# Optimization experiments

Hardware: AMD Instinct MI355X
Metric: run time of the kernel (lower is better)

The kernel has to match this reference:

```python
import jax, jax.numpy as jnp
import numpy as np

HID = 1152      # vision_hidden_size
HEADS = 16      # vision_num_heads
HD = HID // HEADS  # 72
INTER = 4304    # vision_intermediate_size
SEQ = 16384     # total vision tokens
WIN = 64        # tokens per attention window
EPS = 1e-6


def setup_inputs() -> dict:
    key = jax.random.key(0)
    ks = jax.random.split(key, 14)
    f32 = jnp.float32
    x = jax.random.normal(ks[0], (SEQ, HID), f32)
    # RoPE tables: standard rotary angles, full head_dim via concat(ang, ang)
    inv_freq = 1.0 / (10000.0 ** (jnp.arange(0, HD // 2, dtype=f32) / (HD // 2)))
    ang = jnp.arange(SEQ, dtype=f32)[:, None] * inv_freq[None, :]
    emb = jnp.concatenate([ang, ang], axis=-1)          # [SEQ, HD]
    cos, sin = jnp.cos(emb), jnp.sin(emb)
    cu_seqlens = jnp.arange(SEQ // WIN + 1, dtype=jnp.int32) * WIN  # uniform windows
    sc = 0.02
    return {
        "x": x, "cos": cos, "sin": sin, "cu_seqlens": cu_seqlens,
        "qkv_w": jax.random.normal(ks[1], (HID, 3 * HID), f32) * sc,
        "qkv_b": jnp.zeros((3 * HID,), f32),
        "proj_w": jax.random.normal(ks[2], (HID, HID), f32) * sc,
        "proj_b": jnp.zeros((HID,), f32),
        "ln1_w": jnp.ones((HID,), f32), "ln1_b": jnp.zeros((HID,), f32),
        "ln2_w": jnp.ones((HID,), f32), "ln2_b": jnp.zeros((HID,), f32),
        "fc1_w": jax.random.normal(ks[3], (HID, INTER), f32) * sc,
        "fc1_b": jnp.zeros((INTER,), f32),
        "fc2_w": jax.random.normal(ks[4], (INTER, HID), f32) * sc,
        "fc2_b": jnp.zeros((HID,), f32),
    }


def _layer_norm(h, w, b):
    hf = h.astype(jnp.float32)
    mean = jnp.mean(hf, axis=-1, keepdims=True)
    var = jnp.mean((hf - mean) ** 2, axis=-1, keepdims=True)
    return ((hf - mean) * jax.lax.rsqrt(var + EPS)) * w + b


def _rotate_half(t):
    t1, t2 = jnp.split(t, 2, axis=-1)
    return jnp.concatenate((-t2, t1), axis=-1)


def reference(x, cos, sin, cu_seqlens,
              qkv_w, qkv_b, proj_w, proj_b,
              ln1_w, ln1_b, ln2_w, ln2_b,
              fc1_w, fc1_b, fc2_w, fc2_b):
    S = x.shape[0]
    n_win = cu_seqlens.shape[0] - 1
    W = S // n_win  # uniform windows (block-diagonal attention)

    # --- attention branch ---
    h = _layer_norm(x, ln1_w, ln1_b)
    qkv = h @ qkv_w + qkv_b
    q, k, v = jnp.split(qkv, 3, axis=-1)
    q = q.reshape(S, HEADS, HD)
    k = k.reshape(S, HEADS, HD)
    v = v.reshape(S, HEADS, HD)
    c = cos[:, None, :HD]
    s = sin[:, None, :HD]
    q = q * c + _rotate_half(q) * s
    k = k * c + _rotate_half(k) * s
    # block-diagonal windowed attention: [n_win, W, HEADS, HD]
    qw = q.reshape(n_win, W, HEADS, HD).astype(jnp.float32)
    kw = k.reshape(n_win, W, HEADS, HD).astype(jnp.float32)
    vw = v.reshape(n_win, W, HEADS, HD).astype(jnp.float32)
    scores = jnp.einsum('wqhd,wkhd->whqk', qw, kw) * (HD ** -0.5)
    probs = jax.nn.softmax(scores, axis=-1)
    out = jnp.einsum('whqk,wkhd->wqhd', probs, vw).reshape(S, HID)
    x = x + (out @ proj_w + proj_b)

    # --- MLP branch ---
    h2 = _layer_norm(x, ln2_w, ln2_b)
    m = jax.nn.gelu(h2 @ fc1_w + fc1_b, approximate=True)
    return x + (m @ fc2_w + fc2_b)
```

## Files before the change

### kernel.cpp

```cpp
#include <hip/hip_runtime.h>
#include <stdint.h>


#define SEQ   16384
#define HID   1152
#define NH    16
#define HDIM  72
#define INTER 4304
#define INTERP 4352
#define QKVN  3456

using bf16x8 = __attribute__((ext_vector_type(8))) __bf16;
using f32x4  = __attribute__((ext_vector_type(4))) float;

__device__ __forceinline__ float bf2f(uint16_t u){ return __uint_as_float(((uint32_t)u)<<16); }
__device__ __forceinline__ uint16_t f2bf(float f){
  uint32_t u = __float_as_uint(f);
  u += 0x7fffu + ((u>>16)&1u);
  return (uint16_t)(u>>16);
}
__device__ __forceinline__ float gelu_tanh(float x){
  float t = tanhf(0.7978845608028654f*(x + 0.044715f*x*x*x));
  return 0.5f*x*(1.0f + t);
}
__device__ __forceinline__ void async_load16(const void* g, void* l){
  __builtin_amdgcn_global_load_lds((__attribute__((address_space(1))) void*)(void*)g,
                                   (__attribute__((address_space(3))) void*)l, 16, 0, 0);
}

__global__ void transpose_cast(const float* __restrict__ src, uint16_t* __restrict__ dst,
                               int R, int C, int Rp)
{
  __shared__ float tile[32][33];
  const int tx = threadIdx.x & 31, ty = threadIdx.x >> 5;
  const int c = blockIdx.x*32 + tx;
  #pragma unroll
  for (int s = 0; s < 4; ++s){
    const int r = blockIdx.y*32 + ty + s*8;
    tile[ty + s*8][tx] = (r < R && c < C) ? src[(size_t)r*C + c] : 0.0f;
  }
  __syncthreads();
  #pragma unroll
  for (int s = 0; s < 4; ++s){
    const int oc = blockIdx.x*32 + ty + s*8;
    const int orr = blockIdx.y*32 + tx;
    dst[(size_t)oc*Rp + orr] = f2bf(tile[tx][ty + s*8]);
  }
}

__global__ void ln_kernel(const float* __restrict__ x, const float* __restrict__ w,
                          const float* __restrict__ b, uint16_t* __restrict__ out)
{
  const int wid = threadIdx.x >> 6, lane = threadIdx.x & 63;
  const int row = blockIdx.x*4 + wid;
  const float* xr = x + (size_t)row*HID;
  float v[18];
  float s = 0.f;
  #pragma unroll
  for (int t = 0; t < 18; ++t){ v[t] = xr[lane + t*64]; s += v[t]; }
  #pragma unroll
  for (int m = 32; m; m >>= 1) s += __shfl_xor(s, m, 64);
  const float mean = s * (1.0f/HID);
  float q = 0.f;
  #pragma unroll
  for (int t = 0; t < 18; ++t){ float d = v[t]-mean; q += d*d; }
  #pragma unroll
  for (int m = 32; m; m >>= 1) q += __shfl_xor(q, m, 64);
  const float rstd = rsqrtf(q*(1.0f/HID) + 1e-6f);
  uint16_t* orow = out + (size_t)row*HID;
  #pragma unroll
  for (int t = 0; t < 18; ++t){
    const int j = lane + t*64;
    orow[j] = f2bf((v[t]-mean)*rstd*w[j] + b[j]);
  }
}

__global__ void rope_kernel(uint16_t* __restrict__ qkv, const float* __restrict__ cosb,
                            const float* __restrict__ sinb)
{
  const int idx = blockIdx.x*256 + threadIdx.x;
  const int s  = idx / (NH*36);
  const int r1 = idx - s*(NH*36);
  const int h  = r1 / 36;
  const int d  = r1 - h*36;
  const float c  = cosb[s*HDIM + d];
  const float sn = sinb[s*HDIM + d];
  const size_t b = (size_t)s*QKVN + h*HDIM + d;
  float q1 = bf2f(qkv[b]), q2 = bf2f(qkv[b+36]);
  qkv[b]    = f2bf(q1*c - q2*sn);
  qkv[b+36] = f2bf(q2*c + q1*sn);
  float k1 = bf2f(qkv[b+HID]), k2 = bf2f(qkv[b+HID+36]);
  qkv[b+HID]    = f2bf(k1*c - k2*sn);
  qkv[b+HID+36] = f2bf(k2*c + k1*sn);
}

__global__ __launch_bounds__(256,2) void attn_kernel(const uint16_t* __restrict__ qkv,
                                                     uint16_t* __restrict__ outb)
{
  __shared__ float Q[64*76];
  __shared__ float K[64*76];
  __shared__ float V[64*76];
  __shared__ float P[64*68];
  const int tid = threadIdx.x;
  const int win = blockIdx.x >> 4, h = blockIdx.x & 15;
  const size_t base = (size_t)win*64*QKVN + h*HDIM;
  {
    const int r = tid >> 2, q4 = tid & 3;
    const size_t rb = base + (size_t)r*QKVN;
    #pragma unroll
    for (int p0 = 0; p0 < 9; ++p0){
      const int p = q4*9 + p0;
      const uint32_t uq = *(const uint32_t*)(qkv + rb + 2*p);
      const uint32_t uk = *(const uint32_t*)(qkv + rb + HID + 2*p);
      const uint32_t uv = *(const uint32_t*)(qkv + rb + 2*HID + 2*p);
      Q[r*76+2*p] = bf2f((uint16_t)uq); Q[r*76+2*p+1] = bf2f((uint16_t)(uq>>16));
      K[r*76+2*p] = bf2f((uint16_t)uk); K[r*76+2*p+1] = bf2f((uint16_t)(uk>>16));
      V[r*76+2*p] = bf2f((uint16_t)uv); V[r*76+2*p+1] = bf2f((uint16_t)(uv>>16));
    }
  }
  __syncthreads();
  const int rg = tid >> 4, cg = tid & 15;
  const int r0 = rg*4, c0 = cg*4;
  float sc[4][4] = {};
  #pragma unroll 3
  for (int kk = 0; kk < 18; ++kk){
    float4 qv[4], kv[4];
    #pragma unroll
    for (int i = 0; i < 4; ++i) qv[i] = *(const float4*)&Q[(r0+i)*76 + kk*4];
    #pragma unroll
    for (int j = 0; j < 4; ++j) kv[j] = *(const float4*)&K[(c0+j)*76 + kk*4];
    #pragma unroll
    for (int i = 0; i < 4; ++i)
      #pragma unroll
      for (int j = 0; j < 4; ++j)
        sc[i][j] += qv[i].x*kv[j].x + qv[i].y*kv[j].y + qv[i].z*kv[j].z + qv[i].w*kv[j].w;
  }
  const float scale = 0.11785113019775793f;
  #pragma unroll
  for (int i = 0; i < 4; ++i){
    float a0 = sc[i][0]*scale, a1 = sc[i][1]*scale, a2 = sc[i][2]*scale, a3 = sc[i][3]*scale;
    float m = fmaxf(fmaxf(a0,a1), fmaxf(a2,a3));
    m = fmaxf(m, __shfl_xor(m, 1, 16));
    m = fmaxf(m, __shfl_xor(m, 2, 16));
    m = fmaxf(m, __shfl_xor(m, 4, 16));
    m = fmaxf(m, __shfl_xor(m, 8, 16));
    float e0 = __expf(a0-m), e1 = __expf(a1-m), e2 = __expf(a2-m), e3 = __expf(a3-m);
    float sm = e0+e1+e2+e3;
    sm += __shfl_xor(sm, 1, 16);
    sm += __shfl_xor(sm, 2, 16);
    sm += __shfl_xor(sm, 4, 16);
    sm += __shfl_xor(sm, 8, 16);
    const float inv = 1.0f/sm;
    *(float4*)&P[(r0+i)*68 + c0] = make_float4(e0*inv, e1*inv, e2*inv, e3*inv);
  }
  __syncthreads();
  for (int d4 = cg; d4 < 18; d4 += 16){
    float4 o[4] = {};
    #pragma unroll 4
    for (int k4 = 0; k4 < 16; ++k4){
      float4 pr[4];
      #pragma unroll
      for (int i = 0; i < 4; ++i) pr[i] = *(const float4*)&P[(r0+i)*68 + k4*4];
      const float4 v0 = *(const float4*)&V[(k4*4+0)*76 + d4*4];
      const float4 v1 = *(const float4*)&V[(k4*4+1)*76 + d4*4];
      const float4 v2 = *(const float4*)&V[(k4*4+2)*76 + d4*4];
      const float4 v3 = *(const float4*)&V[(k4*4+3)*76 + d4*4];
      #pragma unroll
      for (int i = 0; i < 4; ++i){
        o[i].x += pr[i].x*v0.x + pr[i].y*v1.x + pr[i].z*v2.x + pr[i].w*v3.x;
        o[i].y += pr[i].x*v0.y + pr[i].y*v1.y + pr[i].z*v2.y + pr[i].w*v3.y;
        o[i].z += pr[i].x*v0.z + pr[i].y*v1.z + pr[i].z*v2.z + pr[i].w*v3.z;
        o[i].w += pr[i].x*v0.w + pr[i].y*v1.w + pr[i].z*v2.w + pr[i].w*v3.w;
      }
    }
    #pragma unroll
    for (int i = 0; i < 4; ++i){
      const int token = win*64 + r0 + i;
      const size_t ob = (size_t)token*HID + h*HDIM + d4*4;
      outb[ob+0] = f2bf(o[i].x); outb[ob+1] = f2bf(o[i].y);
      outb[ob+2] = f2bf(o[i].z); outb[ob+3] = f2bf(o[i].w);
    }
  }
}

template<int EPI>
__global__ __launch_bounds__(256,3) void gemm_bt(
    const uint16_t* __restrict__ A, const uint16_t* __restrict__ Bt,
    const float* __restrict__ bias, int Nb,
    const float* res, void* outp, int N, int K, int NB)
{
  __shared__ uint16_t sA[128*64];
  __shared__ uint16_t sB[128*64];
  const int tid = threadIdx.x, wid = tid >> 6, lane = tid & 63;
  const int per  = gridDim.x >> 3;
  const int tile = (blockIdx.x & 7)*per + (blockIdx.x >> 3);
  const int mb   = tile / NB;
  const int mBase = mb*128, nBase = (tile - mb*NB)*128;
  const int wm = wid >> 1, wn = wid & 1;
  const int sr = lane >> 2;
  const int sk = lane & 3;
  const int gk = sk ^ ((sr >> 1) & 3);
  const int rr = lane & 15;
  const int rq = lane >> 4;
  const int rp = rq ^ ((rr >> 1) & 3);
  f32x4 acc[4][4] = {};

  for (int k0 = 0; k0 < K; k0 += 64){
    __syncthreads();
    #pragma unroll
    for (int j = 0; j < 4; ++j){
      const int c  = wid*4 + j;
      const int rc = c >> 1, h = c & 1;
      const size_t gcol = (size_t)(k0 + h*32 + gk*8);
      async_load16(A  + (size_t)(mBase + rc*16 + sr)*K + gcol, &sA[c*512]);
      async_load16(Bt + (size_t)(nBase + rc*16 + sr)*K + gcol, &sB[c*512]);
    }
    __syncthreads();
    #pragma unroll
    for (int h = 0; h < 2; ++h){
      bf16x8 af[4], bfr[4];
      #pragma unroll
      for (int i = 0; i < 4; ++i)
        af[i] = *(const bf16x8*)&sA[((wm*4 + i)*2 + h)*512 + rr*32 + rp*8];
      #pragma unroll
      for (int j = 0; j < 4; ++j)
        bfr[j] = *(const bf16x8*)&sB[((wn*4 + j)*2 + h)*512 + rr*32 + rp*8];
      #pragma unroll
      for (int i = 0; i < 4; ++i)
        #pragma unroll
        for (int j = 0; j < 4; ++j)
          acc[i][j] = __builtin_amdgcn_mfma_f32_16x16x32_bf16(af[i], bfr[j], acc[i][j], 0, 0, 0);
    }
  }

  const int rqd = (lane>>4)*4, cl = lane & 15;
  #pragma unroll
  for (int i = 0; i < 4; ++i){
    #pragma unroll
    for (int j = 0; j < 4; ++j){
      const int col = nBase + wn*64 + j*16 + cl;
      const float bv = (col < Nb) ? bias[col] : 0.0f;
      #pragma unroll
      for (int r = 0; r < 4; ++r){
        const int row = mBase + wm*64 + i*16 + rqd + r;
        const float v = acc[i][j][r] + bv;
        const size_t o = (size_t)row*N + col;
        if (EPI == 0)      ((uint16_t*)outp)[o] = f2bf(v);
        else if (EPI == 1) ((uint16_t*)outp)[o] = f2bf(gelu_tanh(v));
        else               ((float*)outp)[o] = v + res[o];
      }
    }
  }
}

extern "C" void kernel_launch(void* const* d_in, const int* in_sizes, int n_in,
                              void* d_out, int out_size, void* d_ws, size_t ws_size,
                              hipStream_t stream)
{
  const float* x      = (const float*)d_in[0];
  const float* cosb   = (const float*)d_in[1];
  const float* sinb   = (const float*)d_in[2];
  const float* qkv_w  = (const float*)d_in[4];
  const float* qkv_b  = (const float*)d_in[5];
  const float* proj_w = (const float*)d_in[6];
  const float* proj_b = (const float*)d_in[7];
  const float* ln1_w  = (const float*)d_in[8];
  const float* ln1_b  = (const float*)d_in[9];
  const float* ln2_w  = (const float*)d_in[10];
  const float* ln2_b  = (const float*)d_in[11];
  const float* fc1_w  = (const float*)d_in[12];
  const float* fc1_b  = (const float*)d_in[13];
  const float* fc2_w  = (const float*)d_in[14];
  const float* fc2_b  = (const float*)d_in[15];

  char* ws = (char*)d_ws;
  uint16_t* Wqkv  = (uint16_t*)(ws + 0);
  uint16_t* Wproj = (uint16_t*)(ws + 7962624);
  uint16_t* Wfc1  = (uint16_t*)(ws + 10616832);
  uint16_t* Wfc2  = (uint16_t*)(ws + 20643840);
  uint16_t* Hbuf  = (uint16_t*)(ws + 30670848);
  uint16_t* QKV   = (uint16_t*)(ws + 68419584);
  uint16_t* MB    = QKV;
  float* X1 = (float*)d_out;

  transpose_cast<<<dim3(108,36), 256, 0, stream>>>(qkv_w, Wqkv, 1152, 3456, 1152);
  transpose_cast<<<dim3(36,36),  256, 0, stream>>>(proj_w, Wproj, 1152, 1152, 1152);
  transpose_cast<<<dim3(136,36), 256, 0, stream>>>(fc1_w, Wfc1, 1152, 4304, 1152);
  transpose_cast<<<dim3(36,136), 256, 0, stream>>>(fc2_w, Wfc2, 4304, 1152, 4352);

  ln_kernel<<<4096, 256, 0, stream>>>(x, ln1_w, ln1_b, Hbuf);
  gemm_bt<0><<<27*128, 256, 0, stream>>>(Hbuf, Wqkv, qkv_b, QKVN, nullptr, QKV, QKVN, HID, 27);
  rope_kernel<<<36864, 256, 0, stream>>>(QKV, cosb, sinb);
  attn_kernel<<<4096, 256, 0, stream>>>(QKV, Hbuf);
  gemm_bt<2><<<9*128, 256, 0, stream>>>(Hbuf, Wproj, proj_b, HID, x, X1, HID, HID, 9);
  ln_kernel<<<4096, 256, 0, stream>>>(X1, ln2_w, ln2_b, Hbuf);
  gemm_bt<1><<<34*128, 256, 0, stream>>>(Hbuf, Wfc1, fc1_b, INTER, nullptr, MB, INTERP, HID, 34);
  gemm_bt<2><<<9*128, 256, 0, stream>>>(MB, Wfc2, fc2_b, HID, X1, X1, HID, INTERP, 9);
}
```

Before: 1.175 ms.

## Fuse RoPE into attention load, vectorize LayerNorm, use exp2-based GELU

The separate RoPE kernel is removed. Rotary embedding is now applied while Q and K are loaded into shared memory inside the attention kernel, which avoids a full read-modify-write pass over the QKV buffer. LayerNorm now loads and stores with float2 and packs two bf16 values per store. The tanh GELU is rewritten in its equivalent sigmoid form using exp2f, which is mathematically the same but cheaper to compute in the fc1 epilogue. RoPE now sees unrounded bf16 inputs rather than a rounded intermediate, so numerics shift slightly.

After: 1.160 ms. About the same (-1.3%).

```diff
diff --git a/kernel.cpp b/kernel.cpp
--- a/kernel.cpp
+++ b/kernel.cpp
@@ -19,9 +19,9 @@
   u += 0x7fffu + ((u>>16)&1u);
   return (uint16_t)(u>>16);
 }
-__device__ __forceinline__ float gelu_tanh(float x){
-  float t = tanhf(0.7978845608028654f*(x + 0.044715f*x*x*x));
-  return 0.5f*x*(1.0f + t);
+__device__ __forceinline__ float gelu_fast(float x){
+  const float z = 2.3022085f * x * (1.0f + 0.044715f*x*x);
+  return x / (1.0f + exp2f(-z));
 }
 __device__ __forceinline__ void async_load16(const void* g, void* l){
   __builtin_amdgcn_global_load_lds((__attribute__((address_space(1))) void*)(void*)g,
@@ -53,48 +53,39 @@
 {
   const int wid = threadIdx.x >> 6, lane = threadIdx.x & 63;
   const int row = blockIdx.x*4 + wid;
-  const float* xr = x + (size_t)row*HID;
-  float v[18];
+  const float2* xr = (const float2*)(x + (size_t)row*HID);
+  float2 v[9];
   float s = 0.f;
   #pragma unroll
-  for (int t = 0; t < 18; ++t){ v[t] = xr[lane + t*64]; s += v[t]; }
+  for (int t = 0; t < 9; ++t){ v[t] = xr[lane + t*64]; s += v[t].x + v[t].y; }
   #pragma unroll
   for (int m = 32; m; m >>= 1) s += __shfl_xor(s, m, 64);
   const float mean = s * (1.0f/HID);
   float q = 0.f;
   #pragma unroll
-  for (int t = 0; t < 18; ++t){ float d = v[t]-mean; q += d*d; }
+  for (int t = 0; t < 9; ++t){
+    float dx = v[t].x-mean, dy = v[t].y-mean;
+    q += dx*dx + dy*dy;
+  }
   #pragma unroll
   for (int m = 32; m; m >>= 1) q += __shfl_xor(q, m, 64);
   const float rstd = rsqrtf(q*(1.0f/HID) + 1e-6f);
-  uint16_t* orow = out + (size_t)row*HID;
-  #pragma unroll
-  for (int t = 0; t < 18; ++t){
+  const float2* w2 = (const float2*)w;
+  const float2* b2 = (const float2*)b;
+  uint32_t* orow = (uint32_t*)(out + (size_t)row*HID);
+  #pragma unroll
+  for (int t = 0; t < 9; ++t){
     const int j = lane + t*64;
-    orow[j] = f2bf((v[t]-mean)*rstd*w[j] + b[j]);
-  }
-}
-
-__global__ void rope_kernel(uint16_t* __restrict__ qkv, const float* __restrict__ cosb,
-                            const float* __restrict__ sinb)
-{
-  const int idx = blockIdx.x*256 + threadIdx.x;
-  const int s  = idx / (NH*36);
-  const int r1 = idx - s*(NH*36);
-  const int h  = r1 / 36;
-  const int d  = r1 - h*36;
-  const float c  = cosb[s*HDIM + d];
-  const float sn = sinb[s*HDIM + d];
-  const size_t b = (size_t)s*QKVN + h*HDIM + d;
-  float q1 = bf2f(qkv[b]), q2 = bf2f(qkv[b+36]);
-  qkv[b]    = f2bf(q1*c - q2*sn);
-  qkv[b+36] = f2bf(q2*c + q1*sn);
-  float k1 = bf2f(qkv[b+HID]), k2 = bf2f(qkv[b+HID+36]);
-  qkv[b+HID]    = f2bf(k1*c - k2*sn);
-  qkv[b+HID+36] = f2bf(k2*c + k1*sn);
+    const float2 wv = w2[j], bv = b2[j];
+    const float o0 = (v[t].x-mean)*rstd*wv.x + bv.x;
+    const float o1 = (v[t].y-mean)*rstd*wv.y + bv.y;
+    orow[j] = (uint32_t)f2bf(o0) | ((uint32_t)f2bf(o1)<<16);
+  }
 }
 
 __global__ __launch_bounds__(256,2) void attn_kernel(const uint16_t* __restrict__ qkv,
+                                                     const float* __restrict__ cosb,
+                                                     const float* __restrict__ sinb,
                                                      uint16_t* __restrict__ outb)
 {
   __shared__ float Q[64*76];
@@ -107,14 +98,30 @@
   {
     const int r = tid >> 2, q4 = tid & 3;
     const size_t rb = base + (size_t)r*QKVN;
+    const float* crow = cosb + (size_t)(win*64 + r)*HDIM;
+    const float* srow = sinb + (size_t)(win*64 + r)*HDIM;
+    const int isK = q4 >> 1;
+    const size_t mb = rb + (size_t)(isK ? HID : 0);
+    float* dst = isK ? &K[r*76] : &Q[r*76];
+    const int pb = (q4 & 1)*9;
+    #pragma unroll
+    for (int p0 = 0; p0 < 9; ++p0){
+      const int d0 = (pb + p0)*2;
+      const uint32_t ulo = *(const uint32_t*)(qkv + mb + d0);
+      const uint32_t uhi = *(const uint32_t*)(qkv + mb + d0 + 36);
+      const float2 c2 = *(const float2*)(crow + d0);
+      const float2 s2 = *(const float2*)(srow + d0);
+      const float l0 = bf2f((uint16_t)ulo), l1 = bf2f((uint16_t)(ulo>>16));
+      const float h0 = bf2f((uint16_t)uhi), h1 = bf2f((uint16_t)(uhi>>16));
+      dst[d0]    = l0*c2.x - h0*s2.x;
+      dst[d0+1]  = l1*c2.y - h1*s2.y;
+      dst[d0+36] = h0*c2.x + l0*s2.x;
+      dst[d0+37] = h1*c2.y + l1*s2.y;
+    }
     #pragma unroll
     for (int p0 = 0; p0 < 9; ++p0){
       const int p = q4*9 + p0;
-      const uint32_t uq = *(const uint32_t*)(qkv + rb + 2*p);
-      const uint32_t uk = *(const uint32_t*)(qkv + rb + HID + 2*p);
       const uint32_t uv = *(const uint32_t*)(qkv + rb + 2*HID + 2*p);
-      Q[r*76+2*p] = bf2f((uint16_t)uq); Q[r*76+2*p+1] = bf2f((uint16_t)(uq>>16));
-      K[r*76+2*p] = bf2f((uint16_t)uk); K[r*76+2*p+1] = bf2f((uint16_t)(uk>>16));
       V[r*76+2*p] = bf2f((uint16_t)uv); V[r*76+2*p+1] = bf2f((uint16_t)(uv>>16));
     }
   }
@@ -246,7 +253,7 @@
         const float v = acc[i][j][r] + bv;
         const size_t o = (size_t)row*N + col;
         if (EPI == 0)      ((uint16_t*)outp)[o] = f2bf(v);
-        else if (EPI == 1) ((uint16_t*)outp)[o] = f2bf(gelu_tanh(v));
+        else if (EPI == 1) ((uint16_t*)outp)[o] = f2bf(gelu_fast(v));
         else               ((float*)outp)[o] = v + res[o];
       }
     }
@@ -290,8 +297,7 @@
 
   ln_kernel<<<4096, 256, 0, stream>>>(x, ln1_w, ln1_b, Hbuf);
   gemm_bt<0><<<27*128, 256, 0, stream>>>(Hbuf, Wqkv, qkv_b, QKVN, nullptr, QKV, QKVN, HID, 27);
-  rope_kernel<<<36864, 256, 0, stream>>>(QKV, cosb, sinb);
-  attn_kernel<<<4096, 256, 0, stream>>>(QKV, Hbuf);
+  attn_kernel<<<4096, 256, 0, stream>>>(QKV, cosb, sinb, Hbuf);
   gemm_bt<2><<<9*128, 256, 0, stream>>>(Hbuf, Wproj, proj_b, HID, x, X1, HID, HID, 9);
   ln_kernel<<<4096, 256, 0, stream>>>(X1, ln2_w, ln2_b, Hbuf);
   gemm_bt<1><<<34*128, 256, 0, stream>>>(Hbuf, Wfc1, fc1_b, INTER, nullptr, MB, INTERP, HID, 34);
```
